# Performance work log

Hardware: AMD Instinct MI355X
Metric: run time of the kernel (lower is better)

## Reference

```python
import jax, jax.numpy as jnp
import numpy as np

B, Lq, Lk = 2, 4096, 1024
Q_DIM, KV_DIM = 2048, 2048
H, HD = 16, 128          # n_heads, head_dim (nope part)
KVC, QC, R = 512, 768, 64  # kv_comp_dim, q_comp_dim, retr_dim (RoPE part)
LOOKBACK = 8
NEG = -1e30


def setup_inputs() -> dict:
    key = jax.random.key(0)
    ks = jax.random.split(key, 11)
    def w(k, shape, fan_in):
        return jax.random.normal(k, shape, jnp.float32) / np.sqrt(fan_in).astype(np.float32)
    return {
        'q': jax.random.normal(ks[0], (B, Lq, Q_DIM), jnp.float32),
        'kv': jax.random.normal(ks[1], (B, Lk, KV_DIM), jnp.float32),
        'seg_id': jnp.sort(jax.random.randint(ks[2], (B, Lq), 0, Lk), axis=-1),
        'W_kvc': w(ks[3], (KV_DIM, KVC), KV_DIM),   # kv_comp linear (no bias)
        'W_dq':  w(ks[4], (Q_DIM, QC), Q_DIM),      # query down-projection
        'W_uq':  w(ks[5], (QC, H * HD), QC),        # query up-proj (nope)
        'W_qr':  w(ks[6], (QC, H * R), QC),         # query rope proj
        'W_uk':  w(ks[7], (KVC, H * HD), KVC),      # key up-proj (nope)
        'W_kr':  w(ks[8], (KVC, R), KVC),           # shared key rope proj
        'W_uv':  w(ks[9], (KVC, H * HD), KVC),      # value up-proj
        'W_o':   w(ks[10], (H * HD, Q_DIM), H * HD),# output projection
    }


def _rope(x, L):
    # x: [..., L, R] with R even; positions 0..L-1 on the -2 axis.
    half = x.shape[-1] // 2
    inv_freq = 1.0 / (10000.0 ** (jnp.arange(half, dtype=jnp.float32) / half))
    ang = jnp.arange(L, dtype=jnp.float32)[:, None] * inv_freq  # [L, half]
    cos, sin = jnp.cos(ang), jnp.sin(ang)
    x1, x2 = x[..., :half], x[..., half:]
    return jnp.concatenate([x1 * cos - x2 * sin, x1 * sin + x2 * cos], axis=-1)


def reference(q, kv, seg_id, W_kvc, W_dq, W_uq, W_qr, W_uk, W_kr, W_uv, W_o):
    b, lq, _ = q.shape
    lk = kv.shape[1]
    kv_c = kv @ W_kvc                                   # [B,Lk,KVC]
    q_c = q @ W_dq                                      # [B,Lq,QC]
    q_nope = (q_c @ W_uq).reshape(b, lq, H, HD).transpose(0, 2, 1, 3)  # [B,H,Lq,HD]
    q_rope = (q_c @ W_qr).reshape(b, lq, H, R).transpose(0, 2, 1, 3)   # [B,H,Lq,R]
    k_nope = (kv_c @ W_uk).reshape(b, lk, H, HD)        # [B,Lk,H,HD]
    v = (kv_c @ W_uv).reshape(b, lk, H, HD)             # [B,Lk,H,HD]
    k_rope = kv_c @ W_kr                                # [B,Lk,R] shared across heads
    q_rope = _rope(q_rope, lq)
    k_rope = _rope(k_rope, lk)
    scale = 1.0 / np.sqrt(HD + R).astype(np.float32)
    scores = (jnp.einsum('bhqd,bkhd->bhqk', q_nope, k_nope)
              + jnp.einsum('bhqr,bkr->bhqk', q_rope, k_rope)) * scale
    # segment lookback block mask: allow q_seg - lookback <= k <= q_seg
    k_ids = jnp.arange(lk)[None, None, :]               # [1,1,Lk]
    qs = seg_id[:, :, None]                             # [B,Lq,1]
    good = (k_ids <= qs) & (k_ids >= qs - LOOKBACK)     # [B,Lq,Lk]
    scores = jnp.where(good[:, None, :, :], scores, NEG)
    attn = jax.nn.softmax(scores, axis=-1)              # [B,H,Lq,Lk]
    out = jnp.einsum('bhqk,bkhd->bqhd', attn, v).reshape(b, lq, H * HD)
    return out @ W_o                                    # [B,Lq,Q_DIM]
```

## Files before the change

### kernel.cpp

```cpp
#include <hip/hip_runtime.h>
#include <math.h>

typedef __bf16 bf16_t;
typedef __bf16 bf16x8 __attribute__((ext_vector_type(8)));
typedef float f32x4 __attribute__((ext_vector_type(4)));

#define B_    2
#define LQ    4096
#define LK    1024
#define QDIM  2048
#define KVDIM 2048
#define H_    16
#define HD_   128
#define KVC_  512
#define QC_   768
#define R_    64

#define QCOMB 3072
#define KCOMB 4224

typedef __attribute__((address_space(1))) void gvoid_t;
typedef __attribute__((address_space(3))) void lvoid_t;

static __device__ __forceinline__ void gld_lds16(const void* g, void* l) {
  __builtin_amdgcn_global_load_lds((gvoid_t*)(void*)g, (lvoid_t*)l, 16, 0, 0);
}

__global__ void cvt2_f32_bf16(const float* __restrict__ a, bf16_t* __restrict__ oa, long na,
                              const float* __restrict__ b, bf16_t* __restrict__ ob, long nb) {
  const long stride = (long)gridDim.x * blockDim.x * 8;
  for (long i = ((long)blockIdx.x * blockDim.x + threadIdx.x) * 8; i < na; i += stride) {
    float4 x = *(const float4*)(a + i);
    float4 y = *(const float4*)(a + i + 4);
    bf16x8 t;
    t[0] = (bf16_t)x.x; t[1] = (bf16_t)x.y; t[2] = (bf16_t)x.z; t[3] = (bf16_t)x.w;
    t[4] = (bf16_t)y.x; t[5] = (bf16_t)y.y; t[6] = (bf16_t)y.z; t[7] = (bf16_t)y.w;
    *(bf16x8*)(oa + i) = t;
  }
  for (long i = ((long)blockIdx.x * blockDim.x + threadIdx.x) * 8; i < nb; i += stride) {
    float4 x = *(const float4*)(b + i);
    float4 y = *(const float4*)(b + i + 4);
    bf16x8 t;
    t[0] = (bf16_t)x.x; t[1] = (bf16_t)x.y; t[2] = (bf16_t)x.z; t[3] = (bf16_t)x.w;
    t[4] = (bf16_t)y.x; t[5] = (bf16_t)y.y; t[6] = (bf16_t)y.z; t[7] = (bf16_t)y.w;
    *(bf16x8*)(ob + i) = t;
  }
}

struct TransAll {
  const float* src[8];
  bf16_t* dst[8];
  int K[8], N[8], gx[8];
  int off[9];
};

__global__ __launch_bounds__(256) void transpose_all(TransAll d) {
  const int bid = blockIdx.x;
  int i = 0;
#pragma unroll
  for (int j = 1; j < 8; ++j) if (bid >= d.off[j]) i = j;
  const float* __restrict__ src = d.src[i];
  bf16_t* __restrict__ dst = d.dst[i];
  const int K = d.K[i], N = d.N[i];
  const int local = bid - d.off[i];
  const int gx = d.gx[i];
  const int bx = (local % gx) * 32, by = (local / gx) * 32;
  __shared__ float t[32][33];
  const int x = threadIdx.x, y = threadIdx.y;
#pragma unroll
  for (int j = 0; j < 32; j += 8)
    t[y + j][x] = src[(size_t)(by + y + j) * N + bx + x];
  __syncthreads();
#pragma unroll
  for (int j = 0; j < 32; j += 8)
    dst[(size_t)(bx + y + j) * K + by + x] = (bf16_t)t[x][y + j];
}

template <int TN, typename CT>
__device__ __forceinline__ void big2_body(
    const bf16_t* __restrict__ A, const bf16_t* __restrict__ Bt, CT* __restrict__ C,
    int N, int K, int row0, int col0, bf16_t* lA, bf16_t* lB) {
  constexpr int NF = TN / 64;
  constexpr int LW = 4 + TN / 64;
  const int tid = threadIdx.x;
  const int w = tid >> 6, lane = tid & 63;
  const int wm = w >> 2, wn = w & 3;
  const int lr = lane >> 3;
  const int kswz = ((lane & 7) ^ lr) * 8;
  const int nt = K >> 6;
  const int fr = lane & 15, fq = lane >> 4;

  auto STAGE = [&](int t, int buf) {
    const int k0 = t << 6;
#pragma unroll
    for (int j = 0; j < 4; ++j) {
      const int s = j * 8 + w;
      gld_lds16(A + (size_t)(row0 + s * 8 + lr) * K + k0 + kswz, &lA[buf * 256 * 64 + s * 512]);
    }
#pragma unroll
    for (int j = 0; j < TN / 64; ++j) {
      const int s = j * 8 + w;
      gld_lds16(Bt + (size_t)(col0 + s * 8 + lr) * K + k0 + kswz, &lB[buf * TN * 64 + s * 512]);
    }
  };

  bf16x8 aA[8], bA[NF], aB[8], bB[NF];
  f32x4 acc[8][NF];
#pragma unroll
  for (int i = 0; i < 8; ++i)
#pragma unroll
    for (int j = 0; j < NF; ++j) acc[i][j] = f32x4{0.f, 0.f, 0.f, 0.f};

  auto READ = [&](int buf, int kk, bf16x8* a, bf16x8* b) {
    const int swzk = (kk * 32 + fq * 8) ^ ((fr & 7) << 3);
#pragma unroll
    for (int mf = 0; mf < 8; ++mf)
      a[mf] = *(const bf16x8*)&lA[buf * 256 * 64 + (wm * 128 + mf * 16 + fr) * 64 + swzk];
#pragma unroll
    for (int nf = 0; nf < NF; ++nf)
      b[nf] = *(const bf16x8*)&lB[buf * TN * 64 + (wn * (TN / 4) + nf * 16 + fr) * 64 + swzk];
  };
  auto MF = [&](bf16x8* a, bf16x8* b) {
    __builtin_amdgcn_s_setprio(1);
#pragma unroll
    for (int mf = 0; mf < 8; ++mf)
#pragma unroll
      for (int nf = 0; nf < NF; ++nf)
        acc[mf][nf] = __builtin_amdgcn_mfma_f32_16x16x32_bf16(a[mf], b[nf], acc[mf][nf], 0, 0, 0);
    __builtin_amdgcn_s_setprio(0);
  };

  STAGE(0, 0);
  STAGE(1, 1);
  if constexpr (LW == 8) { asm volatile("s_waitcnt vmcnt(8)" ::: "memory"); }
  else                   { asm volatile("s_waitcnt vmcnt(6)" ::: "memory"); }
  __builtin_amdgcn_sched_barrier(0);
  __builtin_amdgcn_s_barrier();
  READ(0, 0, aA, bA);

  for (int t = 0; t < nt; ++t) {
    const int buf = t & 1;
    READ(buf, 1, aB, bB);
    __builtin_amdgcn_sched_barrier(0);
    MF(aA, bA);
    asm volatile("s_waitcnt lgkmcnt(0)" ::: "memory");
    __builtin_amdgcn_sched_barrier(0);
    __builtin_amdgcn_s_barrier();
    if (t + 2 < nt) {
      STAGE(t + 2, buf);
      if constexpr (LW == 8) { asm volatile("s_waitcnt vmcnt(8)" ::: "memory"); }
      else                   { asm volatile("s_waitcnt vmcnt(6)" ::: "memory"); }
    } else {
      asm volatile("s_waitcnt vmcnt(0)" ::: "memory");
    }
    __builtin_amdgcn_sched_barrier(0);
    __builtin_amdgcn_s_barrier();
    if (t + 1 < nt) READ(buf ^ 1, 0, aA, bA);
    __builtin_amdgcn_sched_barrier(0);
    MF(aB, bB);
  }

#pragma unroll
  for (int mf = 0; mf < 8; ++mf)
#pragma unroll
    for (int nf = 0; nf < NF; ++nf) {
      const int col = col0 + wn * (TN / 4) + nf * 16 + fr;
#pragma unroll
      for (int r = 0; r < 4; ++r) {
        const int row = row0 + wm * 128 + mf * 16 + fq * 4 + r;
        C[(size_t)row * N + col] = (CT)acc[mf][nf][r];
      }
    }
}

__global__ __launch_bounds__(512, 2) void gemm_dual(
    const bf16_t* __restrict__ A0, const bf16_t* __restrict__ B0, bf16_t* __restrict__ C0,
    int N0, int K0,
    const bf16_t* __restrict__ A1, const bf16_t* __restrict__ B1, bf16_t* __restrict__ C1,
    int N1, int K1, int split) {
  __shared__ __align__(16) bf16_t lA[2 * 256 * 64];
  __shared__ __align__(16) bf16_t lB[2 * 128 * 64];
  const int nwg = gridDim.x;
  const int orig = blockIdx.x;
  const int wg = (orig & 7) * (nwg >> 3) + (orig >> 3);
  if (wg < split) {
    const int gx = N0 / 128;
    big2_body<128, bf16_t>(A0, B0, C0, N0, K0, (wg / gx) * 256, (wg % gx) * 128, lA, lB);
  } else {
    const int l = wg - split;
    const int gx = N1 / 128;
    big2_body<128, bf16_t>(A1, B1, C1, N1, K1, (l / gx) * 256, (l % gx) * 128, lA, lB);
  }
}

#define SWZK_(ks) (((ks) * 32 + fq * 8) ^ ((fr & 7) << 3))
#define RD_A(buf, q) { _Pragma("unroll") for (int mf = 0; mf < 4; ++mf) { \
    ar[mf][0] = *(const bf16x8*)&sA[((buf) * 2 + wm) * 8192 + ((q) * 64 + mf * 16 + fr) * 64 + SWZK_(0)]; \
    ar[mf][1] = *(const bf16x8*)&sA[((buf) * 2 + wm) * 8192 + ((q) * 64 + mf * 16 + fr) * 64 + SWZK_(1)]; } }
#define RD_B(buf, nq) { _Pragma("unroll") for (int nf = 0; nf < 2; ++nf) { \
    br[nq][nf][0] = *(const bf16x8*)&sB[((buf) * 2 + wbh) * 8192 + (wbr + (nq) * 32 + nf * 16 + fr) * 64 + SWZK_(0)]; \
    br[nq][nf][1] = *(const bf16x8*)&sB[((buf) * 2 + wbh) * 8192 + (wbr + (nq) * 32 + nf * 16 + fr) * 64 + SWZK_(1)]; } }
#define MFMA_Q(mq, nq) { __builtin_amdgcn_s_setprio(1); \
  _Pragma("unroll") for (int mf = 0; mf < 4; ++mf) \
  _Pragma("unroll") for (int nf = 0; nf < 2; ++nf) { \
    acc[(mq)*4+mf][(nq)*2+nf] = __builtin_amdgcn_mfma_f32_16x16x32_bf16(ar[mf][0], br[nq][nf][0], acc[(mq)*4+mf][(nq)*2+nf], 0, 0, 0); \
    acc[(mq)*4+mf][(nq)*2+nf] = __builtin_amdgcn_mfma_f32_16x16x32_bf16(ar[mf][1], br[nq][nf][1], acc[(mq)*4+mf][(nq)*2+nf], 0, 0, 0); } \
  __builtin_amdgcn_s_setprio(0); }
#define SBAR_ __builtin_amdgcn_sched_barrier(0)
#define HBAR_ __builtin_amdgcn_s_barrier()

template <typename CT>
__device__ __forceinline__ void ph8_body(
    const bf16_t* __restrict__ A, const bf16_t* __restrict__ Bt, CT* __restrict__ C,
    int N, int K, int row0, int col0, bf16_t* sA, bf16_t* sB) {
  const int tid = threadIdx.x;
  const int w = tid >> 6, lane = tid & 63;
  const int wm = w >> 2, wn = w & 3;
  const int lr = lane >> 3;
  const int kswz = ((lane & 7) ^ lr) * 8;
  const int nt = K >> 6;
  const int fr = lane & 15, fq = lane >> 4;
  const int wbh = wn >> 1;
  const int wbr = (wn & 1) * 64;

  auto stA = [&](int t, int h, int buf) {
    const bf16_t* g = A + (size_t)(row0 + h * 128 + w * 8 + lr) * K + (t << 6) + kswz;
    gld_lds16(g, sA + (buf * 2 + h) * 8192 + w * 512);
    gld_lds16(g + (size_t)64 * K, sA + (buf * 2 + h) * 8192 + 4096 + w * 512);
  };
  auto stB = [&](int t, int h, int buf) {
    const bf16_t* g = Bt + (size_t)(col0 + h * 128 + w * 8 + lr) * K + (t << 6) + kswz;
    gld_lds16(g, sB + (buf * 2 + h) * 8192 + w * 512);
    gld_lds16(g + (size_t)64 * K, sB + (buf * 2 + h) * 8192 + 4096 + w * 512);
  };

  bf16x8 ar[4][2], br[2][2][2];
  f32x4 acc[8][4];
#pragma unroll
  for (int i = 0; i < 8; ++i)
#pragma unroll
    for (int j = 0; j < 4; ++j) acc[i][j] = f32x4{0.f, 0.f, 0.f, 0.f};

  stA(0, 0, 0); stA(0, 1, 0); stB(0, 0, 0); stB(0, 1, 0);
  stB(1, 0, 1); stB(1, 1, 1);
  asm volatile("s_waitcnt vmcnt(4)" ::: "memory");
  SBAR_; HBAR_;

  for (int t = 0; t < nt; ++t) {
    const int buf = t & 1;
    SBAR_;
    RD_A(buf, 0); RD_B(buf, 0);
    if (t + 1 < nt) stA(t + 1, 0, buf ^ 1);
    SBAR_; HBAR_;
    MFMA_Q(0, 0);
    SBAR_; HBAR_;
    SBAR_;
    RD_B(buf, 1);
    if (t + 1 < nt) stA(t + 1, 1, buf ^ 1);
    SBAR_; HBAR_;
    MFMA_Q(0, 1);
    SBAR_; HBAR_;
    SBAR_;
    RD_A(buf, 1);
    if (t + 2 < nt) stB(t + 2, 0, buf);
    SBAR_; HBAR_;
    MFMA_Q(1, 1);
    SBAR_; HBAR_;
    SBAR_;
    if (t + 2 < nt) {
      stB(t + 2, 1, buf);
      asm volatile("s_waitcnt vmcnt(4)" ::: "memory");
    } else {
      asm volatile("s_waitcnt vmcnt(0)" ::: "memory");
    }
    SBAR_; HBAR_; SBAR_;
    MFMA_Q(1, 0);
    SBAR_; HBAR_;
  }

#pragma unroll
  for (int mfg = 0; mfg < 8; ++mfg)
#pragma unroll
    for (int nfg = 0; nfg < 4; ++nfg) {
      const int col = col0 + wn * 64 + (nfg >> 1) * 32 + (nfg & 1) * 16 + fr;
#pragma unroll
      for (int r = 0; r < 4; ++r) {
        const int row = row0 + wm * 128 + mfg * 16 + fq * 4 + r;
        C[(size_t)row * N + col] = (CT)acc[mfg][nfg][r];
      }
    }
}

template <typename CT>
__global__ __launch_bounds__(512, 2) void gemm_8ph(
    const bf16_t* __restrict__ A, const bf16_t* __restrict__ Bt,
    CT* __restrict__ C, int M, int N, int K) {
  __shared__ __align__(16) bf16_t sA[2 * 2 * 128 * 64];
  __shared__ __align__(16) bf16_t sB[2 * 2 * 128 * 64];
  const int gx = gridDim.x;
  const int nwg = gx * gridDim.y;
  const int orig = blockIdx.y * gx + blockIdx.x;
  const int wg = (orig & 7) * (nwg >> 3) + (orig >> 3);
  const int bx = wg % gx, by = wg / gx;
  ph8_body<CT>(A, Bt, C, N, K, by * 256, bx * 256, sA, sB);
}

__global__ __launch_bounds__(512, 2) void gemm_up_fused(
    const bf16_t* __restrict__ A0, const bf16_t* __restrict__ B0, bf16_t* __restrict__ C0,
    int N0, int K0, int gx0,
    const bf16_t* __restrict__ A1, const bf16_t* __restrict__ B1, bf16_t* __restrict__ C1,
    int N1, int K1, int gx1, int split) {
  __shared__ __align__(16) bf16_t sA[2 * 2 * 128 * 64];
  __shared__ __align__(16) bf16_t sB[2 * 2 * 128 * 64];
  const int nwg = gridDim.x;
  const int orig = blockIdx.x;
  const int wg = (orig & 7) * (nwg >> 3) + (orig >> 3);
  if (wg < split) {
    ph8_body<bf16_t>(A0, B0, C0, N0, K0, (wg / gx0) * 256, (wg % gx0) * 256, sA, sB);
  } else {
    const int l = wg - split;
    big2_body<128, bf16_t>(A1, B1, C1, N1, K1, (l / gx1) * 256, (l % gx1) * 128, sA, sB);
  }
}

#define QROPE_BLOCKS ((B_ * LQ * H_) / 8)
__global__ __launch_bounds__(256) void rope2_kernel(bf16_t* __restrict__ qbase, bf16_t* __restrict__ kvbase) {
  const int bid = blockIdx.x;
  bf16_t* base;
  int tokStride, hshift, posMask;
  long bidl;
  if (bid < QROPE_BLOCKS) { base = qbase; tokStride = QCOMB; hshift = 4; posMask = LQ - 1; bidl = bid; }
  else { base = kvbase; tokStride = KCOMB; hshift = 0; posMask = LK - 1; bidl = bid - QROPE_BLOCKS; }
  const long idx = bidl * 8 + (threadIdx.x >> 5);
  const int i = threadIdx.x & 31;
  const long tok = idx >> hshift;
  const int h = (int)(idx & ((1 << hshift) - 1));
  const int pos = (int)(tok & posMask);
  bf16_t* p = base + tok * (long)tokStride + h * 64;
  const float x1 = (float)p[i], x2 = (float)p[i + 32];
  const float invf = expf(-((float)i * (1.0f / 32.f)) * 9.210340371976184f);
  float sn, cs;
  sincosf((float)pos * invf, &sn, &cs);
  p[i]      = (bf16_t)(x1 * cs - x2 * sn);
  p[i + 32] = (bf16_t)(x1 * sn + x2 * cs);
}

__global__ __launch_bounds__(256) void attn_sparse(
    const bf16_t* __restrict__ qc, const bf16_t* __restrict__ kvc,
    const int* __restrict__ seg, bf16_t* __restrict__ out) {
  const int qrow = blockIdx.x * 4 + (threadIdx.x >> 6);
  const int lane = threadIdx.x & 63;
  const int h = lane >> 2, sub = lane & 3;
  const int b = qrow >> 12;
  const int s = seg[qrow];
  const int kl = max(0, s - 8);
  const float scale = 0.07216878364870322f;

  float qnf[32], qrf[16];
  {
    const bf16_t* p = qc + (size_t)qrow * QCOMB + h * HD_ + sub * 32;
#pragma unroll
    for (int j = 0; j < 4; ++j) {
      bf16x8 t = *(const bf16x8*)(p + j * 8);
#pragma unroll
      for (int e = 0; e < 8; ++e) qnf[j * 8 + e] = (float)t[e];
    }
    const bf16_t* p2 = qc + (size_t)qrow * QCOMB + 2048 + h * R_ + sub * 16;
#pragma unroll
    for (int j = 0; j < 2; ++j) {
      bf16x8 t = *(const bf16x8*)(p2 + j * 8);
#pragma unroll
      for (int e = 0; e < 8; ++e) qrf[j * 8 + e] = (float)t[e];
    }
  }

  float sc[9];
#pragma unroll
  for (int kk = 0; kk < 9; ++kk) {
    const int kx = kl + kk;
    const bf16_t* kb = kvc + (size_t)(b * LK + kx) * KCOMB;
    float d = 0.f;
    const bf16_t* p = kb + h * HD_ + sub * 32;
#pragma unroll
    for (int j = 0; j < 4; ++j) {
      bf16x8 t = *(const bf16x8*)(p + j * 8);
#pragma unroll
      for (int e = 0; e < 8; ++e) d += qnf[j * 8 + e] * (float)t[e];
    }
    const bf16_t* p2 = kb + 4096 + sub * 16;
#pragma unroll
    for (int j = 0; j < 2; ++j) {
      bf16x8 t = *(const bf16x8*)(p2 + j * 8);
#pragma unroll
      for (int e = 0; e < 8; ++e) d += qrf[j * 8 + e] * (float)t[e];
    }
    d += __shfl_xor(d, 1);
    d += __shfl_xor(d, 2);
    sc[kk] = (kx <= s) ? d * scale : -1e30f;
  }
  float m = sc[0];
#pragma unroll
  for (int kk = 1; kk < 9; ++kk) m = fmaxf(m, sc[kk]);
  float sum = 0.f;
#pragma unroll
  for (int kk = 0; kk < 9; ++kk) { const float p = expf(sc[kk] - m); sc[kk] = p; sum += p; }
  const float inv = 1.f / sum;

  float o[32];
#pragma unroll
  for (int j = 0; j < 32; ++j) o[j] = 0.f;
#pragma unroll
  for (int kk = 0; kk < 9; ++kk) {
    const bf16_t* pv = kvc + (size_t)(b * LK + kl + kk) * KCOMB + 2048 + h * HD_ + sub * 32;
    const float p = sc[kk] * inv;
#pragma unroll
    for (int j = 0; j < 4; ++j) {
      bf16x8 t = *(const bf16x8*)(pv + j * 8);
#pragma unroll
      for (int e = 0; e < 8; ++e) o[j * 8 + e] += p * (float)t[e];
    }
  }
  bf16_t* po = out + (size_t)qrow * (H_ * HD_) + h * HD_ + sub * 32;
#pragma unroll
  for (int j = 0; j < 4; ++j) {
    bf16x8 t;
#pragma unroll
    for (int e = 0; e < 8; ++e) t[e] = (bf16_t)o[j * 8 + e];
    *(bf16x8*)(po + j * 8) = t;
  }
}

extern "C" void kernel_launch(void* const* d_in, const int* in_sizes, int n_in,
                              void* d_out, int out_size, void* d_ws, size_t ws_size,
                              hipStream_t stream) {
  const float* q     = (const float*)d_in[0];
  const float* kv    = (const float*)d_in[1];
  const int*   seg   = (const int*)d_in[2];
  const float* W_kvc = (const float*)d_in[3];
  const float* W_dq  = (const float*)d_in[4];
  const float* W_uq  = (const float*)d_in[5];
  const float* W_qr  = (const float*)d_in[6];
  const float* W_uk  = (const float*)d_in[7];
  const float* W_kr  = (const float*)d_in[8];
  const float* W_uv  = (const float*)d_in[9];
  const float* W_o   = (const float*)d_in[10];
  float* out = (float*)d_out;
  (void)in_sizes; (void)n_in; (void)out_size; (void)ws_size;

  char* ws = (char*)d_ws;
  size_t off = 0;
  auto alloc = [&](size_t bytes) {
    char* p = ws + off;
    off = (off + bytes + 255) & ~(size_t)255;
    return p;
  };
  bf16_t* q_bf    = (bf16_t*)alloc((size_t)B_ * LQ * QDIM * 2);
  bf16_t* kv_bf   = (bf16_t*)alloc((size_t)B_ * LK * KVDIM * 2);
  bf16_t* WkvcT   = (bf16_t*)alloc((size_t)KVC_ * KVDIM * 2);
  bf16_t* WdqT    = (bf16_t*)alloc((size_t)QC_ * QDIM * 2);
  bf16_t* WuqrT   = (bf16_t*)alloc((size_t)QCOMB * QC_ * 2);
  bf16_t* WkvT    = (bf16_t*)alloc((size_t)KCOMB * KVC_ * 2);
  bf16_t* WoT     = (bf16_t*)alloc((size_t)QDIM * (H_ * HD_) * 2);
  bf16_t* kv_c    = (bf16_t*)alloc((size_t)B_ * LK * KVC_ * 2);
  bf16_t* q_c     = (bf16_t*)alloc((size_t)B_ * LQ * QC_ * 2);
  bf16_t* q_comb  = (bf16_t*)alloc((size_t)B_ * LQ * QCOMB * 2);
  bf16_t* kv_comb = (bf16_t*)alloc((size_t)B_ * LK * KCOMB * 2);
  bf16_t* attn_o  = q_bf;

  cvt2_f32_bf16<<<4096, 256, 0, stream>>>(q, q_bf, (long)B_ * LQ * QDIM,
                                          kv, kv_bf, (long)B_ * LK * KVDIM);

  {
    TransAll d;
    auto set = [&](int i, const float* s, bf16_t* dt, int K, int N) {
      d.src[i] = s; d.dst[i] = dt; d.K[i] = K; d.N[i] = N; d.gx[i] = N / 32;
    };
    set(0, W_kvc, WkvcT, KVDIM, KVC_);
    set(1, W_dq,  WdqT,  QDIM,  QC_);
    set(2, W_uq,  WuqrT, QC_,   H_ * HD_);
    set(3, W_qr,  WuqrT + (size_t)(H_ * HD_) * QC_, QC_, H_ * R_);
    set(4, W_uk,  WkvT,  KVC_,  H_ * HD_);
    set(5, W_uv,  WkvT + (size_t)(H_ * HD_) * KVC_, KVC_, H_ * HD_);
    set(6, W_kr,  WkvT + (size_t)2 * (H_ * HD_) * KVC_, KVC_, R_);
    set(7, W_o,   WoT,   H_ * HD_, QDIM);
    int acc_off = 0;
    for (int i = 0; i < 8; ++i) {
      d.off[i] = acc_off;
      acc_off += (d.N[i] / 32) * (d.K[i] / 32);
    }
    d.off[8] = acc_off;
    transpose_all<<<acc_off, dim3(32, 8), 0, stream>>>(d);
  }

  gemm_dual<<<224, 512, 0, stream>>>(
      kv_bf, WkvcT, kv_c, KVC_, KVDIM,
      q_bf, WdqT, q_c, QC_, QDIM, 32);

  gemm_up_fused<<<648, 512, 0, stream>>>(
      q_c, WuqrT, q_comb, QCOMB, QC_, QCOMB / 256,
      kv_c, WkvT, kv_comb, KCOMB, KVC_, KCOMB / 128, 384);

  rope2_kernel<<<QROPE_BLOCKS + (B_ * LK) / 8, 256, 0, stream>>>(q_comb + 2048, kv_comb + 4096);

  attn_sparse<<<(B_ * LQ) / 4, 256, 0, stream>>>(q_comb, kv_comb, seg, attn_o);

  gemm_8ph<float><<<dim3(QDIM / 256, (B_ * LQ) / 256), 512, 0, stream>>>(
      attn_o, WoT, out, B_ * LQ, QDIM, H_ * HD_);
}
```

Baseline: 299.1 us.

## Fuse RoPE into up-projection GEMM epilogues and merge conversion with transpose

Removes the separate RoPE kernel. The rotation is now applied in the epilogues of the query and key up-projection GEMMs: in registers for the q tiles, and through an LDS staging buffer for the kv tile that holds the shared rope columns. It also folds the fp32-to-bf16 input conversion into the weight transpose kernel, so the two become one launch. This removes two kernel launches and a read/write pass over the rope columns. In exchange it adds sincos work and an extra barrier to some GEMM epilogue tiles.

```diff
diff --git a/kernel.cpp b/kernel.cpp
--- a/kernel.cpp
+++ b/kernel.cpp
@@ -19,32 +19,13 @@
 #define QCOMB 3072
 #define KCOMB 4224
 
+#define NL_ROPE (-9.210340371976184f / 32.0f)
+
 typedef __attribute__((address_space(1))) void gvoid_t;
 typedef __attribute__((address_space(3))) void lvoid_t;
 
 static __device__ __forceinline__ void gld_lds16(const void* g, void* l) {
   __builtin_amdgcn_global_load_lds((gvoid_t*)(void*)g, (lvoid_t*)l, 16, 0, 0);
-}
-
-__global__ void cvt2_f32_bf16(const float* __restrict__ a, bf16_t* __restrict__ oa, long na,
-                              const float* __restrict__ b, bf16_t* __restrict__ ob, long nb) {
-  const long stride = (long)gridDim.x * blockDim.x * 8;
-  for (long i = ((long)blockIdx.x * blockDim.x + threadIdx.x) * 8; i < na; i += stride) {
-    float4 x = *(const float4*)(a + i);
-    float4 y = *(const float4*)(a + i + 4);
-    bf16x8 t;
-    t[0] = (bf16_t)x.x; t[1] = (bf16_t)x.y; t[2] = (bf16_t)x.z; t[3] = (bf16_t)x.w;
-    t[4] = (bf16_t)y.x; t[5] = (bf16_t)y.y; t[6] = (bf16_t)y.z; t[7] = (bf16_t)y.w;
-    *(bf16x8*)(oa + i) = t;
-  }
-  for (long i = ((long)blockIdx.x * blockDim.x + threadIdx.x) * 8; i < nb; i += stride) {
-    float4 x = *(const float4*)(b + i);
-    float4 y = *(const float4*)(b + i + 4);
-    bf16x8 t;
-    t[0] = (bf16_t)x.x; t[1] = (bf16_t)x.y; t[2] = (bf16_t)x.z; t[3] = (bf16_t)x.w;
-    t[4] = (bf16_t)y.x; t[5] = (bf16_t)y.y; t[6] = (bf16_t)y.z; t[7] = (bf16_t)y.w;
-    *(bf16x8*)(ob + i) = t;
-  }
 }
 
 struct TransAll {
@@ -54,19 +35,44 @@
   int off[9];
 };
 
-__global__ __launch_bounds__(256) void transpose_all(TransAll d) {
+#define NCVT 4096
+__global__ __launch_bounds__(256) void prep_all(
+    const float* __restrict__ qa, bf16_t* __restrict__ oq, long nq,
+    const float* __restrict__ kva, bf16_t* __restrict__ okv, long nkv,
+    TransAll d) {
+  __shared__ float t[32][33];
   const int bid = blockIdx.x;
+  if (bid < NCVT) {
+    const long stride = (long)NCVT * 256 * 8;
+    for (long i = ((long)bid * 256 + threadIdx.x) * 8; i < nq; i += stride) {
+      float4 x = *(const float4*)(qa + i);
+      float4 y = *(const float4*)(qa + i + 4);
+      bf16x8 v;
+      v[0] = (bf16_t)x.x; v[1] = (bf16_t)x.y; v[2] = (bf16_t)x.z; v[3] = (bf16_t)x.w;
+      v[4] = (bf16_t)y.x; v[5] = (bf16_t)y.y; v[6] = (bf16_t)y.z; v[7] = (bf16_t)y.w;
+      *(bf16x8*)(oq + i) = v;
+    }
+    for (long i = ((long)bid * 256 + threadIdx.x) * 8; i < nkv; i += stride) {
+      float4 x = *(const float4*)(kva + i);
+      float4 y = *(const float4*)(kva + i + 4);
+      bf16x8 v;
+      v[0] = (bf16_t)x.x; v[1] = (bf16_t)x.y; v[2] = (bf16_t)x.z; v[3] = (bf16_t)x.w;
+      v[4] = (bf16_t)y.x; v[5] = (bf16_t)y.y; v[6] = (bf16_t)y.z; v[7] = (bf16_t)y.w;
+      *(bf16x8*)(okv + i) = v;
+    }
+    return;
+  }
+  const int tb = bid - NCVT;
   int i = 0;
 #pragma unroll
-  for (int j = 1; j < 8; ++j) if (bid >= d.off[j]) i = j;
+  for (int j = 1; j < 8; ++j) if (tb >= d.off[j]) i = j;
   const float* __restrict__ src = d.src[i];
   bf16_t* __restrict__ dst = d.dst[i];
   const int K = d.K[i], N = d.N[i];
-  const int local = bid - d.off[i];
+  const int local = tb - d.off[i];
   const int gx = d.gx[i];
   const int bx = (local % gx) * 32, by = (local / gx) * 32;
-  __shared__ float t[32][33];
-  const int x = threadIdx.x, y = threadIdx.y;
+  const int x = threadIdx.x & 31, y = threadIdx.x >> 5;
 #pragma unroll
   for (int j = 0; j < 32; j += 8)
     t[y + j][x] = src[(size_t)(by + y + j) * N + bx + x];
@@ -79,7 +85,7 @@
 template <int TN, typename CT>
 __device__ __forceinline__ void big2_body(
     const bf16_t* __restrict__ A, const bf16_t* __restrict__ Bt, CT* __restrict__ C,
-    int N, int K, int row0, int col0, bf16_t* lA, bf16_t* lB) {
+    int N, int K, int row0, int col0, int ropeKCol, bf16_t* lA, bf16_t* lB) {
   constexpr int NF = TN / 64;
   constexpr int LW = 4 + TN / 64;
   const int tid = threadIdx.x;
@@ -160,6 +166,52 @@
     MF(aB, bB);
   }
 
+  if (col0 == ropeKCol) {
+    float* lf = (float*)lA;
+    if (wn < 2) {
+#pragma unroll
+      for (int mf = 0; mf < 8; ++mf)
+#pragma unroll
+        for (int nf = 0; nf < NF; ++nf)
+#pragma unroll
+          for (int r = 0; r < 4; ++r)
+            lf[(wm * 128 + mf * 16 + fq * 4 + r) * 64 + wn * 32 + nf * 16 + fr] = acc[mf][nf][r];
+    }
+    __syncthreads();
+    if (wn < 2) {
+      const float if0 = expf((float)fr * NL_ROPE);
+      const float if1 = expf((float)(fr + 16) * NL_ROPE);
+#pragma unroll
+      for (int mf = 0; mf < 8; ++mf)
+#pragma unroll
+        for (int r = 0; r < 4; ++r) {
+          const int rl = wm * 128 + mf * 16 + fq * 4 + r;
+          const int row = row0 + rl;
+          const float pos = (float)(row & (LK - 1));
+          float s0, c0, s1, c1;
+          sincosf(pos * if0, &s0, &c0);
+          sincosf(pos * if1, &s1, &c1);
+          const float lo0 = lf[rl * 64 + fr],      hi0 = lf[rl * 64 + 32 + fr];
+          const float lo1 = lf[rl * 64 + 16 + fr], hi1 = lf[rl * 64 + 48 + fr];
+          const float v0 = (wn == 0) ? (lo0 * c0 - hi0 * s0) : (lo0 * s0 + hi0 * c0);
+          const float v1 = (wn == 0) ? (lo1 * c1 - hi1 * s1) : (lo1 * s1 + hi1 * c1);
+          C[(size_t)row * N + col0 + wn * 32 + fr]      = (CT)v0;
+          C[(size_t)row * N + col0 + wn * 32 + 16 + fr] = (CT)v1;
+        }
+    } else {
+#pragma unroll
+      for (int mf = 0; mf < 8; ++mf)
+#pragma unroll
+        for (int nf = 0; nf < NF; ++nf) {
+          const int col = col0 + wn * (TN / 4) + nf * 16 + fr;
+#pragma unroll
+          for (int r = 0; r < 4; ++r)
+            C[(size_t)(row0 + wm * 128 + mf * 16 + fq * 4 + r) * N + col] = (CT)acc[mf][nf][r];
+        }
+    }
+    return;
+  }
+
 #pragma unroll
   for (int mf = 0; mf < 8; ++mf)
 #pragma unroll
@@ -185,11 +237,11 @@
   const int wg = (orig & 7) * (nwg >> 3) + (orig >> 3);
   if (wg < split) {
     const int gx = N0 / 128;
-    big2_body<128, bf16_t>(A0, B0, C0, N0, K0, (wg / gx) * 256, (wg % gx) * 128, lA, lB);
+    big2_body<128, bf16_t>(A0, B0, C0, N0, K0, (wg / gx) * 256, (wg % gx) * 128, -1, lA, lB);
   } else {
     const int l = wg - split;
     const int gx = N1 / 128;
-    big2_body<128, bf16_t>(A1, B1, C1, N1, K1, (l / gx) * 256, (l % gx) * 128, lA, lB);
+    big2_body<128, bf16_t>(A1, B1, C1, N1, K1, (l / gx) * 256, (l % gx) * 128, -1, lA, lB);
   }
 }
 
@@ -212,7 +264,7 @@
 template <typename CT>
 __device__ __forceinline__ void ph8_body(
     const bf16_t* __restrict__ A, const bf16_t* __restrict__ Bt, CT* __restrict__ C,
-    int N, int K, int row0, int col0, bf16_t* sA, bf16_t* sB) {
+    int N, int K, int row0, int col0, int ropeCol0, bf16_t* sA, bf16_t* sB) {
   const int tid = threadIdx.x;
   const int w = tid >> 6, lane = tid & 63;
   const int wm = w >> 2, wn = w & 3;
@@ -278,6 +330,29 @@
     SBAR_; HBAR_;
   }
 
+  if (col0 >= ropeCol0) {
+    const float if0 = expf((float)fr * NL_ROPE);
+    const float if1 = expf((float)(fr + 16) * NL_ROPE);
+    const size_t cbase = (size_t)col0 + wn * 64 + fr;
+#pragma unroll
+    for (int mfg = 0; mfg < 8; ++mfg)
+#pragma unroll
+      for (int r = 0; r < 4; ++r) {
+        const int row = row0 + wm * 128 + mfg * 16 + fq * 4 + r;
+        const float pos = (float)(row & (LQ - 1));
+        float s0, c0, s1, c1;
+        sincosf(pos * if0, &s0, &c0);
+        sincosf(pos * if1, &s1, &c1);
+        const float lo0 = acc[mfg][0][r], hi0 = acc[mfg][2][r];
+        const float lo1 = acc[mfg][1][r], hi1 = acc[mfg][3][r];
+        CT* cr = C + (size_t)row * N + cbase;
+        cr[0]  = (CT)(lo0 * c0 - hi0 * s0);
+        cr[16] = (CT)(lo1 * c1 - hi1 * s1);
+        cr[32] = (CT)(lo0 * s0 + hi0 * c0);
+        cr[48] = (CT)(lo1 * s1 + hi1 * c1);
+      }
+    return;
+  }
 #pragma unroll
   for (int mfg = 0; mfg < 8; ++mfg)
 #pragma unroll
@@ -302,7 +377,7 @@
   const int orig = blockIdx.y * gx + blockIdx.x;
   const int wg = (orig & 7) * (nwg >> 3) + (orig >> 3);
   const int bx = wg % gx, by = wg / gx;
-  ph8_body<CT>(A, Bt, C, N, K, by * 256, bx * 256, sA, sB);
+  ph8_body<CT>(A, Bt, C, N, K, by * 256, bx * 256, 1 << 30, sA, sB);
 }
 
 __global__ __launch_bounds__(512, 2) void gemm_up_fused(
@@ -316,33 +391,11 @@
   const int orig = blockIdx.x;
   const int wg = (orig & 7) * (nwg >> 3) + (orig >> 3);
   if (wg < split) {
-    ph8_body<bf16_t>(A0, B0, C0, N0, K0, (wg / gx0) * 256, (wg % gx0) * 256, sA, sB);
+    ph8_body<bf16_t>(A0, B0, C0, N0, K0, (wg / gx0) * 256, (wg % gx0) * 256, 2048, sA, sB);
   } else {
     const int l = wg - split;
-    big2_body<128, bf16_t>(A1, B1, C1, N1, K1, (l / gx1) * 256, (l % gx1) * 128, sA, sB);
-  }
-}
-
-#define QROPE_BLOCKS ((B_ * LQ * H_) / 8)
-__global__ __launch_bounds__(256) void rope2_kernel(bf16_t* __restrict__ qbase, bf16_t* __restrict__ kvbase) {
-  const int bid = blockIdx.x;
-  bf16_t* base;
-  int tokStride, hshift, posMask;
-  long bidl;
-  if (bid < QROPE_BLOCKS) { base = qbase; tokStride = QCOMB; hshift = 4; posMask = LQ - 1; bidl = bid; }
-  else { base = kvbase; tokStride = KCOMB; hshift = 0; posMask = LK - 1; bidl = bid - QROPE_BLOCKS; }
-  const long idx = bidl * 8 + (threadIdx.x >> 5);
-  const int i = threadIdx.x & 31;
-  const long tok = idx >> hshift;
-  const int h = (int)(idx & ((1 << hshift) - 1));
-  const int pos = (int)(tok & posMask);
-  bf16_t* p = base + tok * (long)tokStride + h * 64;
-  const float x1 = (float)p[i], x2 = (float)p[i + 32];
-  const float invf = expf(-((float)i * (1.0f / 32.f)) * 9.210340371976184f);
-  float sn, cs;
-  sincosf((float)pos * invf, &sn, &cs);
-  p[i]      = (bf16_t)(x1 * cs - x2 * sn);
-  p[i + 32] = (bf16_t)(x1 * sn + x2 * cs);
+    big2_body<128, bf16_t>(A1, B1, C1, N1, K1, (l / gx1) * 256, (l % gx1) * 128, 4096, sA, sB);
+  }
 }
 
 __global__ __launch_bounds__(256) void attn_sparse(
@@ -467,9 +520,6 @@
   bf16_t* kv_comb = (bf16_t*)alloc((size_t)B_ * LK * KCOMB * 2);
   bf16_t* attn_o  = q_bf;
 
-  cvt2_f32_bf16<<<4096, 256, 0, stream>>>(q, q_bf, (long)B_ * LQ * QDIM,
-                                          kv, kv_bf, (long)B_ * LK * KVDIM);
-
   {
     TransAll d;
     auto set = [&](int i, const float* s, bf16_t* dt, int K, int N) {
@@ -489,7 +539,8 @@
       acc_off += (d.N[i] / 32) * (d.K[i] / 32);
     }
     d.off[8] = acc_off;
-    transpose_all<<<acc_off, dim3(32, 8), 0, stream>>>(d);
+    prep_all<<<NCVT + acc_off, 256, 0, stream>>>(
+        q, q_bf, (long)B_ * LQ * QDIM, kv, kv_bf, (long)B_ * LK * KVDIM, d);
   }
 
   gemm_dual<<<224, 512, 0, stream>>>(
@@ -500,8 +551,6 @@
       q_c, WuqrT, q_comb, QCOMB, QC_, QCOMB / 256,
       kv_c, WkvT, kv_comb, KCOMB, KVC_, KCOMB / 128, 384);
 
-  rope2_kernel<<<QROPE_BLOCKS + (B_ * LK) / 8, 256, 0, stream>>>(q_comb + 2048, kv_comb + 4096);
-
   attn_sparse<<<(B_ * LQ) / 4, 256, 0, stream>>>(q_comb, kv_comb, seg, attn_o);
 
   gemm_8ph<float><<<dim3(QDIM / 256, (B_ * LQ) / 256), 512, 0, stream>>>(
```

After: 365.9 us. 1.22x slower.
